# Kernel tuning notes

Hardware: AMD Instinct MI355X
Metric: run time of the kernel (lower is better)

The kernel has to match this reference:

```python
import jax, jax.numpy as jnp
import numpy as np

B, T, J = 64, 1024, 22
PARENTS = [0, 0, 1, 2, 3, 0, 5, 6, 7, 0, 9, 10, 11, 12, 11, 14, 15, 16, 11, 18, 19, 20]
SPARSE_JOINTS = [0, 4, 8, 13, 17, 21]
EE = tuple(SPARSE_JOINTS[1:])                       # end effectors (sparse_joints[1:])
NO_SPARSE = tuple(j for j in range(J) if j not in SPARSE_JOINTS)
LAMBDA_EE, LAMBDA_EE_REG = 1.0, 0.1
IDENT_DQ = np.array([1, 0, 0, 0, 0, 0, 0, 0], dtype=np.float32)


def _qconj(q):
    return q * jnp.array([1.0, -1.0, -1.0, -1.0], q.dtype)


def _qmul(a, b):
    aw, ax, ay, az = a[..., 0], a[..., 1], a[..., 2], a[..., 3]
    bw, bx, by, bz = b[..., 0], b[..., 1], b[..., 2], b[..., 3]
    return jnp.stack([
        aw * bw - ax * bx - ay * by - az * bz,
        aw * bx + ax * bw + ay * bz - az * by,
        aw * by - ax * bz + ay * bw + az * bx,
        aw * bz + ax * by - ay * bx + az * bw], axis=-1)


def _qrot(q, v):
    # rotate vector v by unit quaternion q
    qv = q[..., 1:]
    t = 2.0 * jnp.cross(qv, v)
    return v + q[..., :1] * t + jnp.cross(qv, t)


def _qmat(q):
    w, x, y, z = q[..., 0], q[..., 1], q[..., 2], q[..., 3]
    m = jnp.stack([
        1 - 2 * (y * y + z * z), 2 * (x * y - w * z), 2 * (x * z + w * y),
        2 * (x * y + w * z), 1 - 2 * (x * x + z * z), 2 * (y * z - w * x),
        2 * (x * z - w * y), 2 * (y * z + w * x), 1 - 2 * (x * x + y * y)], axis=-1)
    return m.reshape(m.shape[:-1] + (3, 3))


def _denorm_to_dq(x, mean, std, set_root_identity):
    # x: (B, J*8, T) channel-major dual quats -> (B, T, J, 8)
    x = x * std[None, :, None] + mean[None, :, None]
    if set_root_identity:
        x = x.at[:, :8, :].set(jnp.asarray(IDENT_DQ, x.dtype)[None, :, None])
    b, c, t = x.shape
    return x.reshape(b, c // 8, 8, t).transpose(0, 3, 1, 2)


def _local_rot_from_dq(dq):
    # skeleton_from_dual_quat: real part = global rotation; make local via parent gather
    qr = dq[..., :4]
    qr = qr / jnp.linalg.norm(qr, axis=-1, keepdims=True)
    parent = jnp.asarray(PARENTS)
    local = _qmul(_qconj(qr[:, :, parent, :]), qr)   # (B,T,J,4)
    # forward_ik overwrites root local rotation with identity
    local = local.at[:, :, 0, :].set(jnp.array([1.0, 0.0, 0.0, 0.0], dq.dtype))
    return local


def _fk(local_rot, offsets):
    # fk_2: sequential parent-indexed propagation; root global pos is zeros
    rots = [local_rot[:, :, 0]]
    poss = [jnp.zeros(local_rot.shape[:2] + (3,), local_rot.dtype)]
    for j in range(1, J):
        p = PARENTS[j]
        rots.append(_qmul(rots[p], local_rot[:, :, j]))
        poss.append(_qrot(rots[p], offsets[j]) + poss[p])
    grot = jnp.stack(rots, axis=2)          # (B,T,J,4)
    pos = jnp.stack(poss, axis=2)           # (B,T,J,3)
    return pos, _qmat(grot)                  # positions, (B,T,J,3,3) rot matrices


def setup_inputs() -> dict:
    key = jax.random.key(0)
    ks = jax.random.split(key, 7)
    C = J * 8
    return {
        "input": jax.random.normal(ks[0], (B, C, T), jnp.float32),
        "input_ik": jax.random.normal(ks[1], (B, C - 8, T), jnp.float32),
        "input_decoder": jax.random.normal(ks[2], (B, C, T), jnp.float32),
        "target": jax.random.normal(ks[3], (B, C, T), jnp.float32),
        "mean_dqs": 0.1 * jax.random.normal(ks[4], (C,), jnp.float32),
        "std_dqs": 0.5 + 0.5 * jax.random.uniform(ks[5], (C,), jnp.float32),
        "offsets": jax.random.normal(ks[6], (J, 3), jnp.float32),
    }


def reference(input, input_ik, input_decoder, target, mean_dqs, std_dqs, offsets):
    # prepend identity-slot for the root (8 zero channels), then denormalize
    dq_ik = jnp.concatenate([jnp.zeros_like(input_ik[:, :8, :]), input_ik], axis=1)
    dq_ik = _denorm_to_dq(dq_ik, mean_dqs, std_dqs, True)
    dq_dec = _denorm_to_dq(input_decoder, mean_dqs, std_dqs, True)
    dq_tgt = _denorm_to_dq(target, mean_dqs, std_dqs, False)

    r_ik = _local_rot_from_dq(dq_ik)
    r_dec = _local_rot_from_dq(dq_dec)
    r_tgt = _local_rot_from_dq(dq_tgt)

    pos, rm = _fk(r_ik, offsets)
    tpos, trm = _fk(r_tgt, offsets)
    dpos, drm = _fk(r_dec, offsets)

    ee = jnp.asarray(EE)
    ns = jnp.asarray(NO_SPARSE)
    mse = lambda a, b: jnp.mean((a - b) ** 2)
    loss_ee = mse(pos[:, :, ee], tpos[:, :, ee]) + mse(rm[:, :, ee], trm[:, :, ee])
    loss_reg = mse(dpos[:, :, ns], pos[:, :, ns]) + mse(drm[:, :, ns], rm[:, :, ns])
    return loss_ee * LAMBDA_EE + loss_reg * LAMBDA_EE_REG
```

## Files before the change

### kernel.cpp

```cpp
#include <hip/hip_runtime.h>


#define T_DIM 1024

struct Q { float w, x, y, z; };
struct V3 { float x, y, z; };

__device__ __forceinline__ Q qmul(const Q a, const Q b) {
    Q r;
    r.w = a.w*b.w - a.x*b.x - a.y*b.y - a.z*b.z;
    r.x = a.w*b.x + a.x*b.w + a.y*b.z - a.z*b.y;
    r.y = a.w*b.y - a.x*b.z + a.y*b.w + a.z*b.x;
    r.z = a.w*b.z + a.x*b.y - a.y*b.x + a.z*b.w;
    return r;
}

__device__ __forceinline__ V3 qrot(const Q q, const V3 v) {
    float tx = 2.f*(q.y*v.z - q.z*v.y);
    float ty = 2.f*(q.z*v.x - q.x*v.z);
    float tz = 2.f*(q.x*v.y - q.y*v.x);
    V3 r;
    r.x = v.x + q.w*tx + (q.y*tz - q.z*ty);
    r.y = v.y + q.w*ty + (q.z*tx - q.x*tz);
    r.z = v.z + q.w*tz + (q.x*ty - q.y*tx);
    return r;
}

__device__ __forceinline__ V3 v3add(const V3 a, const V3 b) {
    return V3{a.x+b.x, a.y+b.y, a.z+b.z};
}

__device__ __forceinline__ void qmat(const Q q, float m[9]) {
    float xx=q.x*q.x, yy=q.y*q.y, zz=q.z*q.z;
    float xy=q.x*q.y, xz=q.x*q.z, yz=q.y*q.z;
    float wx=q.w*q.x, wy=q.w*q.y, wz=q.w*q.z;
    m[0]=1.f-2.f*(yy+zz); m[1]=2.f*(xy-wz);     m[2]=2.f*(xz+wy);
    m[3]=2.f*(xy+wz);     m[4]=1.f-2.f*(xx+zz); m[5]=2.f*(yz-wx);
    m[6]=2.f*(xz-wy);     m[7]=2.f*(yz+wx);     m[8]=1.f-2.f*(xx+yy);
}

__device__ __forceinline__ float rmdiff2(const Q a, const Q b) {
    float ma[9], mb[9];
    qmat(a, ma); qmat(b, mb);
    float s = 0.f;
#pragma unroll
    for (int i = 0; i < 9; ++i) { float d = ma[i]-mb[i]; s += d*d; }
    return s;
}

__device__ __forceinline__ float pdiff2(const V3 a, const V3 b) {
    float dx=a.x-b.x, dy=a.y-b.y, dz=a.z-b.z;
    return dx*dx+dy*dy+dz*dz;
}

__device__ __forceinline__ Q loadq_norm(const float* __restrict__ p,
                                        const float* __restrict__ sm,
                                        const float* __restrict__ ss) {
    Q q;
    q.w = p[0*T_DIM]*ss[0]+sm[0];
    q.x = p[1*T_DIM]*ss[1]+sm[1];
    q.y = p[2*T_DIM]*ss[2]+sm[2];
    q.z = p[3*T_DIM]*ss[3]+sm[3];
    float inv = rsqrtf(q.w*q.w+q.x*q.x+q.y*q.y+q.z*q.z);
    q.w*=inv; q.x*=inv; q.y*=inv; q.z*=inv;
    return q;
}

struct St { Q rot; V3 pos; };

template<int J, bool EE>
__device__ __forceinline__ void step(
    St& sik, St& sde, St& stg,
    const float* __restrict__ ikp, const float* __restrict__ dep,
    const float* __restrict__ tgp,
    const float* __restrict__ sm, const float* __restrict__ ss,
    const float* __restrict__ so, const Q q0c,
    float& aep, float& aer, float& arp, float& arr)
{
    const int c0 = J*8;
    Q qik = loadq_norm(ikp + (c0-8)*T_DIM, sm+c0, ss+c0);
    Q qde = loadq_norm(dep +  c0   *T_DIM, sm+c0, ss+c0);
    Q qtg = loadq_norm(tgp +  c0   *T_DIM, sm+c0, ss+c0);
    V3 off = { so[3*J], so[3*J+1], so[3*J+2] };
    V3 pik = v3add(qrot(sik.rot, off), sik.pos);
    V3 pde = v3add(qrot(sde.rot, off), sde.pos);
    V3 ptg = v3add(qrot(stg.rot, off), stg.pos);
    Q rtg = qmul(q0c, qtg);
    if (EE) {
        aep += pdiff2(pik, ptg);
        aer += rmdiff2(qik, rtg);
    } else {
        arp += pdiff2(pde, pik);
        arr += rmdiff2(qde, qik);
    }
    sik.rot = qik; sik.pos = pik;
    sde.rot = qde; sde.pos = pde;
    stg.rot = rtg; stg.pos = ptg;
}

__global__ __launch_bounds__(256, 1) void fk_loss_kernel(
    const float* __restrict__ ik, const float* __restrict__ dec,
    const float* __restrict__ tgt, const float* __restrict__ mean,
    const float* __restrict__ stdv, const float* __restrict__ offs,
    float* __restrict__ out)
{
    __shared__ float sm[176], ss[176], so[66];
    __shared__ float swred[4];
    const int tid = threadIdx.x;
    if (tid < 176) { sm[tid] = mean[tid]; ss[tid] = stdv[tid]; }
    if (tid < 66) so[tid] = offs[tid];
    __syncthreads();

    const int p = blockIdx.x * 256 + tid;
    const int b = p >> 10;
    const int t = p & 1023;
    const float* ikp = ik  + (size_t)b * (168*1024) + t;
    const float* dep = dec + (size_t)b * (176*1024) + t;
    const float* tgp = tgt + (size_t)b * (176*1024) + t;

    float aep=0.f, aer=0.f, arp=0.f, arr=0.f;

    Q q0 = loadq_norm(tgp, sm, ss);
    Q q0c = { q0.w, -q0.x, -q0.y, -q0.z };

    const St root = { {1.f,0.f,0.f,0.f}, {0.f,0.f,0.f} };
    St sik, sde, stg;

    sik = root; sde = root; stg = root;
    step<1,false>(sik,sde,stg, ikp,dep,tgp, sm,ss,so, q0c, aep,aer,arp,arr);
    step<2,false>(sik,sde,stg, ikp,dep,tgp, sm,ss,so, q0c, aep,aer,arp,arr);
    step<3,false>(sik,sde,stg, ikp,dep,tgp, sm,ss,so, q0c, aep,aer,arp,arr);
    step<4,true >(sik,sde,stg, ikp,dep,tgp, sm,ss,so, q0c, aep,aer,arp,arr);
    sik = root; sde = root; stg = root;
    step<5,false>(sik,sde,stg, ikp,dep,tgp, sm,ss,so, q0c, aep,aer,arp,arr);
    step<6,false>(sik,sde,stg, ikp,dep,tgp, sm,ss,so, q0c, aep,aer,arp,arr);
    step<7,false>(sik,sde,stg, ikp,dep,tgp, sm,ss,so, q0c, aep,aer,arp,arr);
    step<8,true >(sik,sde,stg, ikp,dep,tgp, sm,ss,so, q0c, aep,aer,arp,arr);
    sik = root; sde = root; stg = root;
    step<9,false> (sik,sde,stg, ikp,dep,tgp, sm,ss,so, q0c, aep,aer,arp,arr);
    step<10,false>(sik,sde,stg, ikp,dep,tgp, sm,ss,so, q0c, aep,aer,arp,arr);
    step<11,false>(sik,sde,stg, ikp,dep,tgp, sm,ss,so, q0c, aep,aer,arp,arr);
    St sik11 = sik, sde11 = sde, stg11 = stg;
    step<12,false>(sik,sde,stg, ikp,dep,tgp, sm,ss,so, q0c, aep,aer,arp,arr);
    step<13,true >(sik,sde,stg, ikp,dep,tgp, sm,ss,so, q0c, aep,aer,arp,arr);
    sik = sik11; sde = sde11; stg = stg11;
    step<14,false>(sik,sde,stg, ikp,dep,tgp, sm,ss,so, q0c, aep,aer,arp,arr);
    step<15,false>(sik,sde,stg, ikp,dep,tgp, sm,ss,so, q0c, aep,aer,arp,arr);
    step<16,false>(sik,sde,stg, ikp,dep,tgp, sm,ss,so, q0c, aep,aer,arp,arr);
    step<17,true >(sik,sde,stg, ikp,dep,tgp, sm,ss,so, q0c, aep,aer,arp,arr);
    sik = sik11; sde = sde11; stg = stg11;
    step<18,false>(sik,sde,stg, ikp,dep,tgp, sm,ss,so, q0c, aep,aer,arp,arr);
    step<19,false>(sik,sde,stg, ikp,dep,tgp, sm,ss,so, q0c, aep,aer,arp,arr);
    step<20,false>(sik,sde,stg, ikp,dep,tgp, sm,ss,so, q0c, aep,aer,arp,arr);
    step<21,true >(sik,sde,stg, ikp,dep,tgp, sm,ss,so, q0c, aep,aer,arp,arr);

    const float BT = 65536.f;
    float loss = aep * (1.0f/(BT*15.f))
               + aer * (1.0f/(BT*45.f))
               + arp * (0.1f/(BT*48.f))
               + arr * (0.1f/(BT*144.f));

#pragma unroll
    for (int o = 32; o > 0; o >>= 1) loss += __shfl_down(loss, o);
    if ((tid & 63) == 0) swred[tid >> 6] = loss;
    __syncthreads();
    if (tid == 0) {
        atomicAdd(out, swred[0]+swred[1]+swred[2]+swred[3]);
    }
}

__global__ void zero_kernel(float* __restrict__ out) {
    if (threadIdx.x == 0) out[0] = 0.f;
}

extern "C" void kernel_launch(void* const* d_in, const int* in_sizes, int n_in,
                              void* d_out, int out_size, void* d_ws, size_t ws_size,
                              hipStream_t stream) {
    const float* ik   = (const float*)d_in[1];
    const float* dec  = (const float*)d_in[2];
    const float* tgt  = (const float*)d_in[3];
    const float* mean = (const float*)d_in[4];
    const float* stdv = (const float*)d_in[5];
    const float* offs = (const float*)d_in[6];
    float* out = (float*)d_out;

    zero_kernel<<<1, 64, 0, stream>>>(out);
    fk_loss_kernel<<<256, 256, 0, stream>>>(ik, dec, tgt, mean, stdv, offs, out);
}
```

Before: 172.5 us.

## Prefetch joint chains into registers and drop shared-memory parameter staging

Result: no change. 171.7 us (-0.5%).

```diff
diff --git a/kernel.cpp b/kernel.cpp
--- a/kernel.cpp
+++ b/kernel.cpp
@@ -5,6 +5,7 @@
 
 struct Q { float w, x, y, z; };
 struct V3 { float x, y, z; };
+struct St { Q rot; V3 pos; };
 
 __device__ __forceinline__ Q qmul(const Q a, const Q b) {
     Q r;
@@ -26,10 +27,6 @@
     return r;
 }
 
-__device__ __forceinline__ V3 v3add(const V3 a, const V3 b) {
-    return V3{a.x+b.x, a.y+b.y, a.z+b.z};
-}
-
 __device__ __forceinline__ void qmat(const Q q, float m[9]) {
     float xx=q.x*q.x, yy=q.y*q.y, zz=q.z*q.z;
     float xy=q.x*q.y, xz=q.x*q.z, yz=q.y*q.z;
@@ -53,35 +50,54 @@
     return dx*dx+dy*dy+dz*dz;
 }
 
-__device__ __forceinline__ Q loadq_norm(const float* __restrict__ p,
-                                        const float* __restrict__ sm,
-                                        const float* __restrict__ ss) {
+__device__ __forceinline__ V3 v3add(const V3 a, const V3 b) {
+    return V3{a.x+b.x, a.y+b.y, a.z+b.z};
+}
+
+__device__ __forceinline__ Q mkq(const float r[4], const int c0,
+                                 const float* __restrict__ mean,
+                                 const float* __restrict__ stdv) {
     Q q;
-    q.w = p[0*T_DIM]*ss[0]+sm[0];
-    q.x = p[1*T_DIM]*ss[1]+sm[1];
-    q.y = p[2*T_DIM]*ss[2]+sm[2];
-    q.z = p[3*T_DIM]*ss[3]+sm[3];
-    float inv = rsqrtf(q.w*q.w+q.x*q.x+q.y*q.y+q.z*q.z);
+    q.w = r[0]*stdv[c0+0] + mean[c0+0];
+    q.x = r[1]*stdv[c0+1] + mean[c0+1];
+    q.y = r[2]*stdv[c0+2] + mean[c0+2];
+    q.z = r[3]*stdv[c0+3] + mean[c0+3];
+    float inv = rsqrtf(q.w*q.w + q.x*q.x + q.y*q.y + q.z*q.z);
     q.w*=inv; q.x*=inv; q.y*=inv; q.z*=inv;
     return q;
 }
 
-struct St { Q rot; V3 pos; };
-
-template<int J, bool EE>
-__device__ __forceinline__ void step(
-    St& sik, St& sde, St& stg,
+template<int J0, int N>
+__device__ __forceinline__ void prefetch_chain(
     const float* __restrict__ ikp, const float* __restrict__ dep,
     const float* __restrict__ tgp,
-    const float* __restrict__ sm, const float* __restrict__ ss,
-    const float* __restrict__ so, const Q q0c,
+    float (*ikr)[4], float (*der)[4], float (*tgr)[4])
+{
+#pragma unroll
+    for (int jj = 0; jj < N; ++jj) {
+        const int j = J0 + jj;
+#pragma unroll
+        for (int c = 0; c < 4; ++c) {
+            ikr[jj][c] = ikp[((j-1)*8 + c)*T_DIM];
+            der[jj][c] = dep[(j*8 + c)*T_DIM];
+            tgr[jj][c] = tgp[(j*8 + c)*T_DIM];
+        }
+    }
+}
+
+template<int J, bool EE>
+__device__ __forceinline__ void stepr(
+    St& sik, St& sde, St& stg,
+    const float ikr[4], const float der[4], const float tgr[4],
+    const float* __restrict__ mean, const float* __restrict__ stdv,
+    const float* __restrict__ offs, const Q q0c,
     float& aep, float& aer, float& arp, float& arr)
 {
     const int c0 = J*8;
-    Q qik = loadq_norm(ikp + (c0-8)*T_DIM, sm+c0, ss+c0);
-    Q qde = loadq_norm(dep +  c0   *T_DIM, sm+c0, ss+c0);
-    Q qtg = loadq_norm(tgp +  c0   *T_DIM, sm+c0, ss+c0);
-    V3 off = { so[3*J], so[3*J+1], so[3*J+2] };
+    Q qik = mkq(ikr, c0, mean, stdv);
+    Q qde = mkq(der, c0, mean, stdv);
+    Q qtg = mkq(tgr, c0, mean, stdv);
+    V3 off = { offs[3*J], offs[3*J+1], offs[3*J+2] };
     V3 pik = v3add(qrot(sik.rot, off), sik.pos);
     V3 pde = v3add(qrot(sde.rot, off), sde.pos);
     V3 ptg = v3add(qrot(stg.rot, off), stg.pos);
@@ -104,13 +120,8 @@
     const float* __restrict__ stdv, const float* __restrict__ offs,
     float* __restrict__ out)
 {
-    __shared__ float sm[176], ss[176], so[66];
     __shared__ float swred[4];
     const int tid = threadIdx.x;
-    if (tid < 176) { sm[tid] = mean[tid]; ss[tid] = stdv[tid]; }
-    if (tid < 66) so[tid] = offs[tid];
-    __syncthreads();
-
     const int p = blockIdx.x * 256 + tid;
     const int b = p >> 10;
     const int t = p & 1023;
@@ -120,39 +131,60 @@
 
     float aep=0.f, aer=0.f, arp=0.f, arr=0.f;
 
-    Q q0 = loadq_norm(tgp, sm, ss);
-    Q q0c = { q0.w, -q0.x, -q0.y, -q0.z };
-
+    float Aik[4][4], Ade[4][4], Atg[4][4];
+    float Bik[4][4], Bde[4][4], Btg[4][4];
+    float Cik[5][4], Cde[5][4], Ctg[5][4];
+    float Dik[4][4], Dde[4][4], Dtg[4][4];
+    float Eik[4][4], Ede[4][4], Etg[4][4];
+    float rq0[4];
+
+#pragma unroll
+    for (int c = 0; c < 4; ++c) rq0[c] = tgp[c*T_DIM];
+    prefetch_chain<1,4>(ikp, dep, tgp, Aik, Ade, Atg);
+    prefetch_chain<5,4>(ikp, dep, tgp, Bik, Bde, Btg);
+
+    Q q0 = mkq(rq0, 0, mean, stdv);
+    const Q q0c = { q0.w, -q0.x, -q0.y, -q0.z };
     const St root = { {1.f,0.f,0.f,0.f}, {0.f,0.f,0.f} };
     St sik, sde, stg;
 
     sik = root; sde = root; stg = root;
-    step<1,false>(sik,sde,stg, ikp,dep,tgp, sm,ss,so, q0c, aep,aer,arp,arr);
-    step<2,false>(sik,sde,stg, ikp,dep,tgp, sm,ss,so, q0c, aep,aer,arp,arr);
-    step<3,false>(sik,sde,stg, ikp,dep,tgp, sm,ss,so, q0c, aep,aer,arp,arr);
-    step<4,true >(sik,sde,stg, ikp,dep,tgp, sm,ss,so, q0c, aep,aer,arp,arr);
+    stepr<1,false>(sik,sde,stg, Aik[0],Ade[0],Atg[0], mean,stdv,offs, q0c, aep,aer,arp,arr);
+    stepr<2,false>(sik,sde,stg, Aik[1],Ade[1],Atg[1], mean,stdv,offs, q0c, aep,aer,arp,arr);
+    stepr<3,false>(sik,sde,stg, Aik[2],Ade[2],Atg[2], mean,stdv,offs, q0c, aep,aer,arp,arr);
+    stepr<4,true >(sik,sde,stg, Aik[3],Ade[3],Atg[3], mean,stdv,offs, q0c, aep,aer,arp,arr);
+
+    prefetch_chain<9,5>(ikp, dep, tgp, Cik, Cde, Ctg);
+
     sik = root; sde = root; stg = root;
-    step<5,false>(sik,sde,stg, ikp,dep,tgp, sm,ss,so, q0c, aep,aer,arp,arr);
-    step<6,false>(sik,sde,stg, ikp,dep,tgp, sm,ss,so, q0c, aep,aer,arp,arr);
-    step<7,false>(sik,sde,stg, ikp,dep,tgp, sm,ss,so, q0c, aep,aer,arp,arr);
-    step<8,true >(sik,sde,stg, ikp,dep,tgp, sm,ss,so, q0c, aep,aer,arp,arr);
+    stepr<5,false>(sik,sde,stg, Bik[0],Bde[0],Btg[0], mean,stdv,offs, q0c, aep,aer,arp,arr);
+    stepr<6,false>(sik,sde,stg, Bik[1],Bde[1],Btg[1], mean,stdv,offs, q0c, aep,aer,arp,arr);
+    stepr<7,false>(sik,sde,stg, Bik[2],Bde[2],Btg[2], mean,stdv,offs, q0c, aep,aer,arp,arr);
+    stepr<8,true >(sik,sde,stg, Bik[3],Bde[3],Btg[3], mean,stdv,offs, q0c, aep,aer,arp,arr);
+
+    prefetch_chain<14,4>(ikp, dep, tgp, Dik, Dde, Dtg);
+
     sik = root; sde = root; stg = root;
-    step<9,false> (sik,sde,stg, ikp,dep,tgp, sm,ss,so, q0c, aep,aer,arp,arr);
-    step<10,false>(sik,sde,stg, ikp,dep,tgp, sm,ss,so, q0c, aep,aer,arp,arr);
-    step<11,false>(sik,sde,stg, ikp,dep,tgp, sm,ss,so, q0c, aep,aer,arp,arr);
-    St sik11 = sik, sde11 = sde, stg11 = stg;
-    step<12,false>(sik,sde,stg, ikp,dep,tgp, sm,ss,so, q0c, aep,aer,arp,arr);
-    step<13,true >(sik,sde,stg, ikp,dep,tgp, sm,ss,so, q0c, aep,aer,arp,arr);
+    stepr<9, false>(sik,sde,stg, Cik[0],Cde[0],Ctg[0], mean,stdv,offs, q0c, aep,aer,arp,arr);
+    stepr<10,false>(sik,sde,stg, Cik[1],Cde[1],Ctg[1], mean,stdv,offs, q0c, aep,aer,arp,arr);
+    stepr<11,false>(sik,sde,stg, Cik[2],Cde[2],Ctg[2], mean,stdv,offs, q0c, aep,aer,arp,arr);
+    const St sik11 = sik, sde11 = sde, stg11 = stg;
+    stepr<12,false>(sik,sde,stg, Cik[3],Cde[3],Ctg[3], mean,stdv,offs, q0c, aep,aer,arp,arr);
+    stepr<13,true >(sik,sde,stg, Cik[4],Cde[4],Ctg[4], mean,stdv,offs, q0c, aep,aer,arp,arr);
+
+    prefetch_chain<18,4>(ikp, dep, tgp, Eik, Ede, Etg);
+
     sik = sik11; sde = sde11; stg = stg11;
-    step<14,false>(sik,sde,stg, ikp,dep,tgp, sm,ss,so, q0c, aep,aer,arp,arr);
-    step<15,false>(sik,sde,stg, ikp,dep,tgp, sm,ss,so, q0c, aep,aer,arp,arr);
-    step<16,false>(sik,sde,stg, ikp,dep,tgp, sm,ss,so, q0c, aep,aer,arp,arr);
-    step<17,true >(sik,sde,stg, ikp,dep,tgp, sm,ss,so, q0c, aep,aer,arp,arr);
+    stepr<14,false>(sik,sde,stg, Dik[0],Dde[0],Dtg[0], mean,stdv,offs, q0c, aep,aer,arp,arr);
+    stepr<15,false>(sik,sde,stg, Dik[1],Dde[1],Dtg[1], mean,stdv,offs, q0c, aep,aer,arp,arr);
+    stepr<16,false>(sik,sde,stg, Dik[2],Dde[2],Dtg[2], mean,stdv,offs, q0c, aep,aer,arp,arr);
+    stepr<17,true >(sik,sde,stg, Dik[3],Dde[3],Dtg[3], mean,stdv,offs, q0c, aep,aer,arp,arr);
+
     sik = sik11; sde = sde11; stg = stg11;
-    step<18,false>(sik,sde,stg, ikp,dep,tgp, sm,ss,so, q0c, aep,aer,arp,arr);
-    step<19,false>(sik,sde,stg, ikp,dep,tgp, sm,ss,so, q0c, aep,aer,arp,arr);
-    step<20,false>(sik,sde,stg, ikp,dep,tgp, sm,ss,so, q0c, aep,aer,arp,arr);
-    step<21,true >(sik,sde,stg, ikp,dep,tgp, sm,ss,so, q0c, aep,aer,arp,arr);
+    stepr<18,false>(sik,sde,stg, Eik[0],Ede[0],Etg[0], mean,stdv,offs, q0c, aep,aer,arp,arr);
+    stepr<19,false>(sik,sde,stg, Eik[1],Ede[1],Etg[1], mean,stdv,offs, q0c, aep,aer,arp,arr);
+    stepr<20,false>(sik,sde,stg, Eik[2],Ede[2],Etg[2], mean,stdv,offs, q0c, aep,aer,arp,arr);
+    stepr<21,true >(sik,sde,stg, Eik[3],Ede[3],Etg[3], mean,stdv,offs, q0c, aep,aer,arp,arr);
 
     const float BT = 65536.f;
     float loss = aep * (1.0f/(BT*15.f))
@@ -169,14 +201,10 @@
     }
 }
 
-__global__ void zero_kernel(float* __restrict__ out) {
-    if (threadIdx.x == 0) out[0] = 0.f;
-}
-
 extern "C" void kernel_launch(void* const* d_in, const int* in_sizes, int n_in,
                               void* d_out, int out_size, void* d_ws, size_t ws_size,
                               hipStream_t stream) {
-    const float* ik   = (const float*)d_in[1];
+    const float* ikx  = (const float*)d_in[1];
     const float* dec  = (const float*)d_in[2];
     const float* tgt  = (const float*)d_in[3];
     const float* mean = (const float*)d_in[4];
@@ -184,6 +212,6 @@
     const float* offs = (const float*)d_in[6];
     float* out = (float*)d_out;
 
-    zero_kernel<<<1, 64, 0, stream>>>(out);
-    fk_loss_kernel<<<256, 256, 0, stream>>>(ik, dec, tgt, mean, stdv, offs, out);
-}
+    hipMemsetAsync(out, 0, sizeof(float), stream);
+    fk_loss_kernel<<<256, 256, 0, stream>>>(ikx, dec, tgt, mean, stdv, offs, out);
+}
```
